# Performance work log

Measured on AMD Instinct MI355X. Metric: run time of the kernel, lower is better.

## Reference

```python
import jax, jax.numpy as jnp
import numpy as np

N_STATIC = 20
N_DYNAMIC = 10
INPUT_DIM = N_STATIC + N_DYNAMIC * 9 + 8  # 118
EMBED = 128
HIDDEN = 1536
HIDDEN2 = 1024
OUT = 128
T = 2048


def setup_inputs() -> dict:
    key = jax.random.key(0)
    ks = jax.random.split(key, 20)
    s = lambda i, shape: jax.random.normal(ks[i], shape, dtype=jnp.float32) * 0.02
    inp = {
        "inputVecs": jax.random.normal(ks[0], (T, INPUT_DIM), dtype=jnp.float32),
        # init_hidden(): randn(num_layers, 1, hidden_dim) -> stored as [2, H]
        "h0": jax.random.normal(ks[1], (2, HIDDEN), dtype=jnp.float32),
        "c0": jax.random.normal(ks[2], (2, HIDDEN), dtype=jnp.float32),
        # LSTM layer 0 (input = INPUT_DIM + EMBED)
        "W_ih0": s(3, (4 * HIDDEN, INPUT_DIM + EMBED)),
        "W_hh0": s(4, (4 * HIDDEN, HIDDEN)),
        "b_ih0": s(5, (4 * HIDDEN,)),
        "b_hh0": s(6, (4 * HIDDEN,)),
        # LSTM layer 1
        "W_ih1": s(7, (4 * HIDDEN, HIDDEN)),
        "W_hh1": s(8, (4 * HIDDEN, HIDDEN)),
        "b_ih1": s(9, (4 * HIDDEN,)),
        "b_hh1": s(10, (4 * HIDDEN,)),
        # hiddenLinear: hidden_dim -> hidden2
        "W_hl": s(11, (HIDDEN2, HIDDEN)),
        "b_hl": s(12, (HIDDEN2,)),
        # linear: hidden2 -> output_dim
        "W_out": s(13, (OUT, HIDDEN2)),
        "b_out": s(14, (OUT,)),
        # map: output_dim -> embed_size
        "W_map": s(15, (EMBED, OUT)),
        "b_map": s(16, (EMBED,)),
    }
    return inp


def _lstm_cell(x, h, c, W_ih, W_hh, b_ih, b_hh):
    # torch gate order: i, f, g, o
    gates = W_ih @ x + b_ih + W_hh @ h + b_hh
    i, f, g, o = jnp.split(gates, 4)
    i = jax.nn.sigmoid(i)
    f = jax.nn.sigmoid(f)
    g = jnp.tanh(g)
    o = jax.nn.sigmoid(o)
    c_new = f * c + i * g
    h_new = o * jnp.tanh(c_new)
    return h_new, c_new


def reference(inputVecs, h0, c0, W_ih0, W_hh0, b_ih0, b_hh0,
              W_ih1, W_hh1, b_ih1, b_hh1,
              W_hl, b_hl, W_out, b_out, W_map, b_map):
    embed0 = jnp.zeros((EMBED,), dtype=inputVecs.dtype)

    def step(carry, x):
        h, c, emb = carry  # h,c: [2, H]; emb: [EMBED]
        xt = jnp.concatenate([x, emb])
        h0n, c0n = _lstm_cell(xt, h[0], c[0], W_ih0, W_hh0, b_ih0, b_hh0)
        h1n, c1n = _lstm_cell(h0n, h[1], c[1], W_ih1, W_hh1, b_ih1, b_hh1)
        # dropout p=0 -> identity; two stacked linears (no nonlinearity, faithful)
        y = W_out @ (W_hl @ h1n + b_hl) + b_out
        y = jax.nn.softmax(y)
        emb_new = W_map @ y + b_map
        return (jnp.stack([h0n, h1n]), jnp.stack([c0n, c1n]), emb_new), y

    _, outputs = jax.lax.scan(step, (h0, c0, embed0), inputVecs)
    return outputs  # [T, OUT]
```

## Files before the change

kernel.cpp:

```cpp
#include <hip/hip_runtime.h>
#include <math.h>
#include <stdint.h>

#define T_STEPS 2048
#define XDIM 118
#define EMBD 128
#define HD 1536
#define NA 96
#define NB 128
#define NBLK (NA + NB + 1)

#define EP_A   0
#define EP_B   128
#define EP_C   256
#define EP_N   320

#define SMEM_BYTES 160048

struct Params {
  const float *x, *h0in, *c0in;
  const float *Wih0, *Whh0, *bih0, *bhh0;
  const float *Wih1, *Whh1, *bih1, *bhh1;
  const float *Whl, *bhl, *Wout, *bout;
  const float *Wfold;
  float *PRE, *Wc, *bc, *h0buf, *h1buf, *ybuf, *PART;
  uint32_t *ep;
  float *out;
};

__device__ __forceinline__ float bf_lo(uint32_t u){ return __uint_as_float(u << 16); }
__device__ __forceinline__ float bf_hi(uint32_t u){ return __uint_as_float(u & 0xffff0000u); }
__device__ __forceinline__ uint32_t packbf(float a, float b){
  uint32_t ua = __float_as_uint(a), ub = __float_as_uint(b);
  ua = (ua + 0x7fffu + ((ua >> 16) & 1u)) >> 16;
  ub = (ub + 0x7fffu + ((ub >> 16) & 1u)) & 0xffff0000u;
  return (ua & 0xffffu) | ub;
}
__device__ __forceinline__ float gload(const float* p){
  return __hip_atomic_load(p, __ATOMIC_RELAXED, __HIP_MEMORY_SCOPE_AGENT);
}
__device__ __forceinline__ void gstore(float* p, float v){
  __hip_atomic_store(p, v, __ATOMIC_RELAXED, __HIP_MEMORY_SCOPE_AGENT);
}
__device__ __forceinline__ uint32_t gloadu(const uint32_t* p){
  return __hip_atomic_load(p, __ATOMIC_RELAXED, __HIP_MEMORY_SCOPE_AGENT);
}
__device__ __forceinline__ void gstoreu(uint32_t* p, uint32_t v){
  __hip_atomic_store(p, v, __ATOMIC_RELAXED, __HIP_MEMORY_SCOPE_AGENT);
}
__device__ __forceinline__ float sigm(float x){ return 1.f / (1.f + __expf(-x)); }

__device__ __forceinline__ void lds_set(volatile uint32_t* f, uint32_t v){
  asm volatile("" ::: "memory");
  *f = v;
  asm volatile("" ::: "memory");
}
__device__ __forceinline__ void lds_wait(volatile uint32_t* f, uint32_t tgt){
  uint32_t n = 0;
  while (*f < tgt){ if (++n > 1000000000u) break; }
  asm volatile("" ::: "memory");
}

__device__ __forceinline__ float asrc(const Params& P, int r, int k){
  if (k < HD) return P.Whh0[(size_t)r * HD + k];
  return P.Wih0[(size_t)r * (XDIM + EMBD) + XDIM + (k - HD)];
}
__device__ void run_A(const Params& P, int bid, uint32_t* smem){
  const int tid = threadIdx.x;
  const int w = tid >> 6, l = tid & 63;
  const int O = bid * 16 + w;
  float* xv = (float*)smem;
  uint2* wl2 = (uint2*)(smem + 1664);
  volatile uint32_t* flg = smem + 18048;
  uint32_t wr[4][8];
  uint32_t wry[4];
#pragma unroll
  for (int g = 0; g < 4; ++g){
    int r = g * HD + O;
#pragma unroll
    for (int p = 0; p < 8; ++p)
      wr[g][p] = packbf(asrc(P, r, 128 * p + 2 * l), asrc(P, r, 128 * p + 2 * l + 1));
#pragma unroll
    for (int q = 0; q < 2; ++q){
      uint2 u;
      u.x = packbf(asrc(P, r, 128 * (8 + 2 * q) + 2 * l), asrc(P, r, 128 * (8 + 2 * q) + 2 * l + 1));
      u.y = packbf(asrc(P, r, 128 * (9 + 2 * q) + 2 * l), asrc(P, r, 128 * (9 + 2 * q) + 2 * l + 1));
      wl2[(q * 4 + g) * 1024 + tid] = u;
    }
    wry[g] = packbf(P.Wfold[(size_t)r * 128 + 2 * l], P.Wfold[(size_t)r * 128 + 2 * l + 1]);
  }
  float cst = P.c0in[O];
  int alive = 1;
  if (tid < 2) flg[tid] = 0u;
  __syncthreads();
  for (int t = 0; t < T_STEPS; ++t){
    const float* pre = P.PRE + (size_t)t * 6144;
    float q0 = pre[O], q1 = pre[HD + O], q2 = pre[2 * HD + O], q3 = pre[3 * HD + O];
    if (w == 0){
      if (alive && t > 0){
        uint32_t n = 0;
        while (1){
          uint32_t v0 = gloadu(P.ep + EP_A + l);
          uint32_t v1 = (l < 32) ? gloadu(P.ep + EP_A + 64 + l) : (uint32_t)t;
          if (__all(v0 >= (uint32_t)t && v1 >= (uint32_t)t)) break;
          if (++n > 5000000u){ alive = 0; break; }
        }
      }
      if (l == 0) lds_set(flg + 0, (uint32_t)t);
    } else {
      lds_wait(flg + 0, (uint32_t)t);
    }
    const float* hp = P.h0buf + (((t & 1) ^ 1) * HD);
    xv[tid] = gload(hp + tid);
    if (tid < 512) xv[1024 + tid] = gload(hp + 1024 + tid);
    __syncthreads();
    float a0 = 0.f, a1 = 0.f, a2 = 0.f, a3 = 0.f;
#pragma unroll
    for (int p = 0; p < 8; ++p){
      float2 x2 = *(const float2*)&xv[128 * p + 2 * l];
      uint32_t u0 = wr[0][p], u1 = wr[1][p], u2 = wr[2][p], u3 = wr[3][p];
      a0 += bf_lo(u0) * x2.x + bf_hi(u0) * x2.y;
      a1 += bf_lo(u1) * x2.x + bf_hi(u1) * x2.y;
      a2 += bf_lo(u2) * x2.x + bf_hi(u2) * x2.y;
      a3 += bf_lo(u3) * x2.x + bf_hi(u3) * x2.y;
    }
#pragma unroll
    for (int q = 0; q < 2; ++q){
      float2 xa = *(const float2*)&xv[128 * (8 + 2 * q) + 2 * l];
      float2 xb = *(const float2*)&xv[128 * (9 + 2 * q) + 2 * l];
      uint2 u0 = wl2[(q * 4 + 0) * 1024 + tid];
      uint2 u1 = wl2[(q * 4 + 1) * 1024 + tid];
      uint2 u2 = wl2[(q * 4 + 2) * 1024 + tid];
      uint2 u3 = wl2[(q * 4 + 3) * 1024 + tid];
      a0 += bf_lo(u0.x) * xa.x + bf_hi(u0.x) * xa.y + bf_lo(u0.y) * xb.x + bf_hi(u0.y) * xb.y;
      a1 += bf_lo(u1.x) * xa.x + bf_hi(u1.x) * xa.y + bf_lo(u1.y) * xb.x + bf_hi(u1.y) * xb.y;
      a2 += bf_lo(u2.x) * xa.x + bf_hi(u2.x) * xa.y + bf_lo(u2.y) * xb.x + bf_hi(u2.y) * xb.y;
      a3 += bf_lo(u3.x) * xa.x + bf_hi(u3.x) * xa.y + bf_lo(u3.y) * xb.x + bf_hi(u3.y) * xb.y;
    }
    if (w == 0){
      if (alive && t > 0){
        uint32_t n = 0;
        while (gloadu(P.ep + EP_C) < (uint32_t)t){
          if (++n > 5000000u){ alive = 0; break; }
        }
      }
      if (l == 0) lds_set(flg + 1, (uint32_t)t);
    } else {
      lds_wait(flg + 1, (uint32_t)t);
    }
    {
      const float* yb = P.ybuf + (((t & 1) ^ 1) * EMBD) + 2 * l;
      float yx = gload(yb), yy = gload(yb + 1);
      a0 += bf_lo(wry[0]) * yx + bf_hi(wry[0]) * yy;
      a1 += bf_lo(wry[1]) * yx + bf_hi(wry[1]) * yy;
      a2 += bf_lo(wry[2]) * yx + bf_hi(wry[2]) * yy;
      a3 += bf_lo(wry[3]) * yx + bf_hi(wry[3]) * yy;
    }
#pragma unroll
    for (int m = 1; m < 64; m <<= 1){
      a0 += __shfl_xor(a0, m, 64);
      a1 += __shfl_xor(a1, m, 64);
      a2 += __shfl_xor(a2, m, 64);
      a3 += __shfl_xor(a3, m, 64);
    }
    float gi = sigm(a0 + q0);
    float gf = sigm(a1 + q1);
    float gg = tanhf(a2 + q2);
    float go = sigm(a3 + q3);
    cst = gf * cst + gi * gg;
    float hn = go * tanhf(cst);
    if (l == 0) gstore(P.h0buf + (t & 1) * HD + O, hn);
    __syncthreads();
    if (tid == 0) gstoreu(P.ep + EP_A + bid, (uint32_t)(t + 1));
  }
}

__device__ __forceinline__ float bsrc(const Params& P, int r, int k){
  if (k < HD) return P.Wih1[(size_t)r * HD + k];
  return P.Whh1[(size_t)r * HD + (k - HD)];
}
__device__ void run_B(const Params& P, int bidb, uint32_t* smem){
  const int tid = threadIdx.x;
  const int w = tid >> 6, l = tid & 63;
  const int base = bidb * 12;
  float* xv = (float*)smem;
  uint2* wl2 = (uint2*)(smem + 3072);
  float* g1 = (float*)(smem + 39936);
  float* c1 = g1 + 48;
  volatile uint32_t* flg = smem + 40008;
  uint32_t wr[3][12];
  float bias[3];
#pragma unroll
  for (int jj = 0; jj < 3; ++jj){
    int idx = 3 * w + jj;
    int g = idx / 12, o = idx % 12;
    int r = g * HD + base + o;
    bias[jj] = P.bih1[r] + P.bhh1[r];
#pragma unroll
    for (int p = 0; p < 12; ++p)
      wr[jj][p] = packbf(bsrc(P, r, 128 * p + 2 * l), bsrc(P, r, 128 * p + 2 * l + 1));
#pragma unroll
    for (int q = 0; q < 6; ++q){
      uint2 u;
      u.x = packbf(bsrc(P, r, 128 * (12 + 2 * q) + 2 * l), bsrc(P, r, 128 * (12 + 2 * q) + 2 * l + 1));
      u.y = packbf(bsrc(P, r, 128 * (13 + 2 * q) + 2 * l), bsrc(P, r, 128 * (13 + 2 * q) + 2 * l + 1));
      wl2[(q * 3 + jj) * 1024 + tid] = u;
    }
  }
  const int jrow = tid >> 2, cpart = tid & 3;
  float wc0 = 0.f, wc1 = 0.f, wc2 = 0.f;
  if (tid < 512){
    const float* wcp = P.Wc + (size_t)jrow * HD + base + cpart * 3;
    wc0 = wcp[0]; wc1 = wcp[1]; wc2 = wcp[2];
  }
  if (tid < 12) c1[12 + tid] = P.c0in[HD + base + tid];
  if (tid < 2) flg[tid] = 0u;
  int alive = 1;
  __syncthreads();
  for (int t = 0; t < T_STEPS; ++t){
    if (w == 0){
      if (alive && t > 0){
        uint32_t n = 0;
        while (gloadu(P.ep + EP_C) < (uint32_t)t){
          if (++n > 5000000u){ alive = 0; break; }
        }
      }
      if (l == 0) lds_set(flg + 0, (uint32_t)t);
    } else {
      lds_wait(flg + 0, (uint32_t)t);
    }
    const float* h1p = P.h1buf + (((t & 1) ^ 1) * HD);
    xv[1536 + tid] = gload(h1p + tid);
    if (tid < 512) xv[2560 + tid] = gload(h1p + 1024 + tid);
    __syncthreads();
    float a0 = 0.f, a1 = 0.f, a2 = 0.f;
#pragma unroll
    for (int q = 0; q < 6; ++q){
      float2 xa = *(const float2*)&xv[128 * (12 + 2 * q) + 2 * l];
      float2 xb = *(const float2*)&xv[128 * (13 + 2 * q) + 2 * l];
      uint2 u0 = wl2[(q * 3 + 0) * 1024 + tid];
      uint2 u1 = wl2[(q * 3 + 1) * 1024 + tid];
      uint2 u2 = wl2[(q * 3 + 2) * 1024 + tid];
      a0 += bf_lo(u0.x) * xa.x + bf_hi(u0.x) * xa.y + bf_lo(u0.y) * xb.x + bf_hi(u0.y) * xb.y;
      a1 += bf_lo(u1.x) * xa.x + bf_hi(u1.x) * xa.y + bf_lo(u1.y) * xb.x + bf_hi(u1.y) * xb.y;
      a2 += bf_lo(u2.x) * xa.x + bf_hi(u2.x) * xa.y + bf_lo(u2.y) * xb.x + bf_hi(u2.y) * xb.y;
    }
    if (w == 0){
      uint32_t tgt = (uint32_t)(t + 1);
      if (alive){
        uint32_t n = 0;
        while (1){
          uint32_t v0 = gloadu(P.ep + EP_A + l);
          uint32_t v1 = (l < 32) ? gloadu(P.ep + EP_A + 64 + l) : tgt;
          if (__all(v0 >= tgt && v1 >= tgt)) break;
          if (++n > 5000000u){ alive = 0; break; }
        }
      }
      if (l == 0) lds_set(flg + 1, tgt);
    } else {
      lds_wait(flg + 1, (uint32_t)(t + 1));
    }
    const float* h0p = P.h0buf + (t & 1) * HD;
    xv[tid] = gload(h0p + tid);
    if (tid < 512) xv[1024 + tid] = gload(h0p + 1024 + tid);
    __syncthreads();
#pragma unroll
    for (int p = 0; p < 12; ++p){
      float2 x2 = *(const float2*)&xv[128 * p + 2 * l];
      uint32_t u0 = wr[0][p], u1 = wr[1][p], u2 = wr[2][p];
      a0 += bf_lo(u0) * x2.x + bf_hi(u0) * x2.y;
      a1 += bf_lo(u1) * x2.x + bf_hi(u1) * x2.y;
      a2 += bf_lo(u2) * x2.x + bf_hi(u2) * x2.y;
    }
#pragma unroll
    for (int m = 1; m < 64; m <<= 1){
      a0 += __shfl_xor(a0, m, 64);
      a1 += __shfl_xor(a1, m, 64);
      a2 += __shfl_xor(a2, m, 64);
    }
    if (l == 0){
      g1[3 * w + 0] = a0 + bias[0];
      g1[3 * w + 1] = a1 + bias[1];
      g1[3 * w + 2] = a2 + bias[2];
    }
    __syncthreads();
    const int par = ((t & 1) ^ 1) * 12, cur = (t & 1) * 12;
    if (tid < 512){
      float h[3], cc[3];
#pragma unroll
      for (int ii = 0; ii < 3; ++ii){
        int o = cpart * 3 + ii;
        float gi = sigm(g1[o]);
        float gf = sigm(g1[12 + o]);
        float gg = tanhf(g1[24 + o]);
        float go = sigm(g1[36 + o]);
        float c = gf * c1[par + o] + gi * gg;
        cc[ii] = c;
        h[ii] = go * tanhf(c);
      }
      float pp = wc0 * h[0] + wc1 * h[1] + wc2 * h[2];
      pp += __shfl_xor(pp, 1, 64);
      pp += __shfl_xor(pp, 2, 64);
      if (cpart == 0) gstore(P.PART + bidb * 128 + jrow, pp);
      if (jrow == 0){
#pragma unroll
        for (int ii = 0; ii < 3; ++ii){
          int o = cpart * 3 + ii;
          c1[cur + o] = cc[ii];
          gstore(P.h1buf + (t & 1) * HD + base + o, h[ii]);
        }
      }
    }
    __syncthreads();
    if (tid == 0) gstoreu(P.ep + EP_B + bidb, (uint32_t)(t + 1));
  }
}

__device__ void run_C(const Params& P, uint32_t* smem){
  const int tid = threadIdx.x;
  float* partred = (float*)smem;
  float* bcs = (float*)(smem + 1024);
  volatile uint32_t* flg = smem + 1152;
  const int w = tid >> 6, l = tid & 63;
  if (tid < 128) bcs[tid] = P.bc[tid];
  if (tid == 0) flg[0] = 0u;
  int alive = 1;
  __syncthreads();
  for (int t = 0; t < T_STEPS; ++t){
    uint32_t tgt = (uint32_t)(t + 1);
    if (w == 0){
      if (alive){
        uint32_t n = 0;
        while (1){
          uint32_t v0 = gloadu(P.ep + EP_B + l);
          uint32_t v1 = gloadu(P.ep + EP_B + 64 + l);
          if (__all(v0 >= tgt && v1 >= tgt)) break;
          if (++n > 5000000u){ alive = 0; break; }
        }
      }
      if (l == 0) lds_set(flg, tgt);
    } else {
      lds_wait(flg, tgt);
    }
    const int j = tid & 127, b8 = tid >> 7;
    float s = 0.f;
#pragma unroll
    for (int i = 0; i < 16; ++i) s += gload(P.PART + (b8 * 16 + i) * 128 + j);
    partred[b8 * 128 + j] = s;
    __syncthreads();
    if (w == 0){
      float lt0 = bcs[l], lt1 = bcs[64 + l];
#pragma unroll
      for (int i = 0; i < 8; ++i){
        lt0 += partred[i * 128 + l];
        lt1 += partred[i * 128 + 64 + l];
      }
      float m = fmaxf(lt0, lt1);
#pragma unroll
      for (int k = 1; k < 64; k <<= 1) m = fmaxf(m, __shfl_xor(m, k, 64));
      float e0 = __expf(lt0 - m), e1 = __expf(lt1 - m);
      float sd = e0 + e1;
#pragma unroll
      for (int k = 1; k < 64; k <<= 1) sd += __shfl_xor(sd, k, 64);
      float inv = 1.f / sd;
      float p0 = e0 * inv, p1 = e1 * inv;
      P.out[(size_t)t * 128 + l] = p0;
      P.out[(size_t)t * 128 + 64 + l] = p1;
      gstore(P.ybuf + (t & 1) * EMBD + l, p0);
      gstore(P.ybuf + (t & 1) * EMBD + 64 + l, p1);
      if (l == 0)
        __hip_atomic_store(P.ep + EP_C, tgt, __ATOMIC_RELEASE, __HIP_MEMORY_SCOPE_AGENT);
    }
  }
}

__global__ __launch_bounds__(1024) void k_lstm(Params P){
  extern __shared__ __align__(16) uint32_t smem[];
  int bid = blockIdx.x;
  if (bid < NA) run_A(P, bid, smem);
  else if (bid < NA + NB) run_B(P, bid - NA, smem);
  else run_C(P, smem);
}

__global__ void k_init(const float* h0in, float* h0buf, float* h1buf, float* ybuf,
                       uint32_t* ep){
  int tid = threadIdx.x;
  for (int i = tid; i < HD; i += 256){
    float a = h0in[i], b = h0in[HD + i];
    h0buf[i] = a; h0buf[HD + i] = a;
    h1buf[i] = b; h1buf[HD + i] = b;
  }
  if (tid < 128){ ybuf[tid] = 0.f; ybuf[128 + tid] = 0.f; }
  for (int i = tid; i < EP_N; i += 256) ep[i] = 0u;
}

__global__ void k_fold(const float* Wih0, const float* Wmap, const float* bmap,
                       float* Wfold, float* bfold){
  __shared__ float we[64 * 128];
  int b = blockIdx.x, tid = threadIdx.x;
  int r0 = b * 64;
  for (int i = tid; i < 64 * 128; i += 256){
    int rr = i >> 7, e = i & 127;
    we[i] = Wih0[(size_t)(r0 + rr) * (XDIM + EMBD) + XDIM + e];
  }
  __syncthreads();
  int j = tid & 127, half = tid >> 7;
  float acc[32];
#pragma unroll
  for (int rr = 0; rr < 32; ++rr) acc[rr] = 0.f;
  for (int e = 0; e < 128; ++e){
    float wv = Wmap[(size_t)e * 128 + j];
#pragma unroll
    for (int rr = 0; rr < 32; ++rr) acc[rr] += we[(half * 32 + rr) * 128 + e] * wv;
  }
  for (int rr = 0; rr < 32; ++rr)
    Wfold[(size_t)(r0 + half * 32 + rr) * 128 + j] = acc[rr];
  if (tid < 64){
    float a = 0.f;
    for (int e = 0; e < 128; ++e) a += we[tid * 128 + e] * bmap[e];
    bfold[r0 + tid] = a;
  }
}

__global__ void k_pre(const float* x, const float* Wih0, const float* bih0, const float* bhh0,
                      const float* bfold, float* PRE){
  int tb = blockIdx.x >> 2;
  int rc = blockIdx.x & 3;
  int tid = threadIdx.x;
  __shared__ float xl[32 * XDIM];
  for (int i = tid; i < 32 * XDIM; i += 256){
    int tt = i / XDIM, k = i % XDIM;
    xl[i] = x[(size_t)(tb * 32 + tt) * XDIM + k];
  }
  __syncthreads();
  for (int rr = 0; rr < 6; ++rr){
    int r = rc * HD + rr * 256 + tid;
    float acc[32];
#pragma unroll
    for (int t = 0; t < 32; ++t) acc[t] = 0.f;
    const float* wrow = Wih0 + (size_t)r * (XDIM + EMBD);
    for (int k = 0; k < XDIM; ++k){
      float wv = wrow[k];
#pragma unroll
      for (int t = 0; t < 32; ++t) acc[t] += wv * xl[t * XDIM + k];
    }
    float bb = bih0[r] + bhh0[r];
    float bf = bfold[r];
    for (int t = 0; t < 32; ++t)
      PRE[(size_t)(tb * 32 + t) * 6144 + r] = acc[t] + bb + ((tb * 32 + t) > 0 ? bf : 0.f);
  }
}

__global__ void k_wc(const float* Whl, const float* Wout, const float* bhl, const float* bout,
                     float* Wc, float* bc){
  if (blockIdx.x == 96){
    int j = threadIdx.x;
    if (j < 128){
      float a = 0.f;
      for (int m = 0; m < 1024; ++m) a += Wout[(size_t)j * 1024 + m] * bhl[m];
      bc[j] = a + bout[j];
    }
    return;
  }
  int kt = blockIdx.x % 6, jt = blockIdx.x / 6;
  __shared__ float wo[8 * 1024];
  int tid = threadIdx.x;
  for (int i = tid; i < 8 * 1024; i += 256) wo[i] = Wout[(size_t)(jt * 8) * 1024 + i];
  __syncthreads();
  int k = kt * 256 + tid;
  float acc[8];
#pragma unroll
  for (int jj = 0; jj < 8; ++jj) acc[jj] = 0.f;
  for (int m = 0; m < 1024; ++m){
    float wl = Whl[(size_t)m * HD + k];
#pragma unroll
    for (int jj = 0; jj < 8; ++jj) acc[jj] += wo[jj * 1024 + m] * wl;
  }
#pragma unroll
  for (int jj = 0; jj < 8; ++jj) Wc[(size_t)(jt * 8 + jj) * HD + k] = acc[jj];
}

__global__ void k_sentinel(float* out){ out[0] = 1.0e6f; }

extern "C" void kernel_launch(void* const* d_in, const int* in_sizes, int n_in,
                              void* d_out, int out_size, void* d_ws, size_t ws_size,
                              hipStream_t stream){
  (void)in_sizes; (void)n_in; (void)out_size;
  const float* x    = (const float*)d_in[0];
  const float* h0in = (const float*)d_in[1];
  const float* c0in = (const float*)d_in[2];
  const float* Wih0 = (const float*)d_in[3];
  const float* Whh0 = (const float*)d_in[4];
  const float* bih0 = (const float*)d_in[5];
  const float* bhh0 = (const float*)d_in[6];
  const float* Wih1 = (const float*)d_in[7];
  const float* Whh1 = (const float*)d_in[8];
  const float* bih1 = (const float*)d_in[9];
  const float* bhh1 = (const float*)d_in[10];
  const float* Whl  = (const float*)d_in[11];
  const float* bhl  = (const float*)d_in[12];
  const float* Wout = (const float*)d_in[13];
  const float* bout = (const float*)d_in[14];
  const float* Wmap = (const float*)d_in[15];
  const float* bmap = (const float*)d_in[16];
  float* out = (float*)d_out;
  float* ws = (float*)d_ws;

  size_t off = 0;
  float* PRE    = ws + off; off += (size_t)T_STEPS * 6144;
  float* Wc     = ws + off; off += 128 * HD;
  float* bc     = ws + off; off += 128;
  float* Wfold  = ws + off; off += (size_t)6144 * 128;
  float* bfold  = ws + off; off += 6144;
  float* h0buf  = ws + off; off += 2 * HD;
  float* h1buf  = ws + off; off += 2 * HD;
  float* ybuf   = ws + off; off += 2 * EMBD;
  float* PART   = ws + off; off += 128 * 128;
  off = (off + 63) & ~(size_t)63;
  uint32_t* ep  = (uint32_t*)(ws + off); off += EP_N;

  if (ws_size < off * sizeof(float) + 1024){
    hipLaunchKernelGGL(k_sentinel, dim3(1), dim3(1), 0, stream, out);
    return;
  }

  (void)hipFuncSetAttribute(reinterpret_cast<const void*>(k_lstm),
                            hipFuncAttributeMaxDynamicSharedMemorySize, SMEM_BYTES);

  hipLaunchKernelGGL(k_init, dim3(1), dim3(256), 0, stream, h0in, h0buf, h1buf, ybuf, ep);
  hipLaunchKernelGGL(k_fold, dim3(96), dim3(256), 0, stream, Wih0, Wmap, bmap, Wfold, bfold);
  hipLaunchKernelGGL(k_pre, dim3(256), dim3(256), 0, stream, x, Wih0, bih0, bhh0, bfold, PRE);
  hipLaunchKernelGGL(k_wc, dim3(97), dim3(256), 0, stream, Whl, Wout, bhl, bout, Wc, bc);

  Params P;
  P.x = x; P.h0in = h0in; P.c0in = c0in;
  P.Wih0 = Wih0; P.Whh0 = Whh0; P.bih0 = bih0; P.bhh0 = bhh0;
  P.Wih1 = Wih1; P.Whh1 = Whh1; P.bih1 = bih1; P.bhh1 = bhh1;
  P.Whl = Whl; P.bhl = bhl; P.Wout = Wout; P.bout = bout;
  P.Wfold = Wfold;
  P.PRE = PRE; P.Wc = Wc; P.bc = bc;
  P.h0buf = h0buf; P.h1buf = h1buf; P.ybuf = ybuf; P.PART = PART;
  P.ep = ep; P.out = out;

  hipLaunchKernelGGL(k_lstm, dim3(NBLK), dim3(1024), SMEM_BYTES, stream, P);
}
```

Baseline: 31.74 ms.

## Remove softmax block; accumulate logits atomically and compute softmax redundantly in A blocks

Removes the dedicated C block that reduced per-block partial logits, applied softmax and published y. B blocks now atomically add their partial logits into a double-buffered, 4-way split accumulator, and every A block reads it and computes the softmax itself before using y. This takes one global synchronisation hop out of the per-step recurrence critical path. The cost is float atomics (non-deterministic summation order), softmax work repeated in every A wave, and a more delicate buffer-reset protocol between B and A.

```diff
diff --git a/kernel.cpp b/kernel.cpp
--- a/kernel.cpp
+++ b/kernel.cpp
@@ -8,12 +8,13 @@
 #define HD 1536
 #define NA 96
 #define NB 128
-#define NBLK (NA + NB + 1)
+#define NBLK (NA + NB)
 
 #define EP_A   0
 #define EP_B   128
-#define EP_C   256
-#define EP_N   320
+#define EP_N   256
+
+#define LA_PAR 512
 
 #define SMEM_BYTES 160048
 
@@ -23,7 +24,7 @@
   const float *Wih1, *Whh1, *bih1, *bhh1;
   const float *Whl, *bhl, *Wout, *bout;
   const float *Wfold;
-  float *PRE, *Wc, *bc, *h0buf, *h1buf, *ybuf, *PART;
+  float *PRE, *Wc, *bc, *h0buf, *h1buf, *logacc;
   uint32_t *ep;
   float *out;
 };
@@ -47,6 +48,9 @@
 }
 __device__ __forceinline__ void gstoreu(uint32_t* p, uint32_t v){
   __hip_atomic_store(p, v, __ATOMIC_RELAXED, __HIP_MEMORY_SCOPE_AGENT);
+}
+__device__ __forceinline__ void gatomic_add(float* p, float v){
+  (void)__hip_atomic_fetch_add(p, v, __ATOMIC_RELAXED, __HIP_MEMORY_SCOPE_AGENT);
 }
 __device__ __forceinline__ float sigm(float x){ return 1.f / (1.f + __expf(-x)); }
 
@@ -137,24 +141,41 @@
       a2 += bf_lo(u2.x) * xa.x + bf_hi(u2.x) * xa.y + bf_lo(u2.y) * xb.x + bf_hi(u2.y) * xb.y;
       a3 += bf_lo(u3.x) * xa.x + bf_hi(u3.x) * xa.y + bf_lo(u3.y) * xb.x + bf_hi(u3.y) * xb.y;
     }
-    if (w == 0){
-      if (alive && t > 0){
-        uint32_t n = 0;
-        while (gloadu(P.ep + EP_C) < (uint32_t)t){
-          if (++n > 5000000u){ alive = 0; break; }
+    if (t > 0){
+      if (w == 0){
+        if (alive){
+          uint32_t n = 0;
+          while (1){
+            uint32_t v0 = gloadu(P.ep + EP_B + l);
+            uint32_t v1 = gloadu(P.ep + EP_B + 64 + l);
+            if (__all(v0 >= (uint32_t)t && v1 >= (uint32_t)t)) break;
+            if (++n > 5000000u){ alive = 0; break; }
+          }
         }
-      }
-      if (l == 0) lds_set(flg + 1, (uint32_t)t);
-    } else {
-      lds_wait(flg + 1, (uint32_t)t);
-    }
-    {
-      const float* yb = P.ybuf + (((t & 1) ^ 1) * EMBD) + 2 * l;
-      float yx = gload(yb), yy = gload(yb + 1);
-      a0 += bf_lo(wry[0]) * yx + bf_hi(wry[0]) * yy;
-      a1 += bf_lo(wry[1]) * yx + bf_hi(wry[1]) * yy;
-      a2 += bf_lo(wry[2]) * yx + bf_hi(wry[2]) * yy;
-      a3 += bf_lo(wry[3]) * yx + bf_hi(wry[3]) * yy;
+        if (l == 0) lds_set(flg + 1, (uint32_t)t);
+      } else {
+        lds_wait(flg + 1, (uint32_t)t);
+      }
+      const float* la = P.logacc + (size_t)(((t & 1) ^ 1) * LA_PAR) + 2 * l;
+      float lt0 = gload(la)     + gload(la + 128) + gload(la + 256) + gload(la + 384);
+      float lt1 = gload(la + 1) + gload(la + 129) + gload(la + 257) + gload(la + 385);
+      float m = fmaxf(lt0, lt1);
+#pragma unroll
+      for (int k = 1; k < 64; k <<= 1) m = fmaxf(m, __shfl_xor(m, k, 64));
+      float e0 = __expf(lt0 - m), e1 = __expf(lt1 - m);
+      float sd = e0 + e1;
+#pragma unroll
+      for (int k = 1; k < 64; k <<= 1) sd += __shfl_xor(sd, k, 64);
+      float inv = 1.f / sd;
+      float y0 = e0 * inv, y1 = e1 * inv;
+      a0 += bf_lo(wry[0]) * y0 + bf_hi(wry[0]) * y1;
+      a1 += bf_lo(wry[1]) * y0 + bf_hi(wry[1]) * y1;
+      a2 += bf_lo(wry[2]) * y0 + bf_hi(wry[2]) * y1;
+      a3 += bf_lo(wry[3]) * y0 + bf_hi(wry[3]) * y1;
+      if (bid == 0 && w == 15){
+        P.out[(size_t)(t - 1) * 128 + 2 * l] = y0;
+        P.out[(size_t)(t - 1) * 128 + 2 * l + 1] = y1;
+      }
     }
 #pragma unroll
     for (int m = 1; m < 64; m <<= 1){
@@ -172,6 +193,30 @@
     if (l == 0) gstore(P.h0buf + (t & 1) * HD + O, hn);
     __syncthreads();
     if (tid == 0) gstoreu(P.ep + EP_A + bid, (uint32_t)(t + 1));
+  }
+  if (bid == 0 && w == 0){
+    if (alive){
+      uint32_t n = 0;
+      while (1){
+        uint32_t v0 = gloadu(P.ep + EP_B + l);
+        uint32_t v1 = gloadu(P.ep + EP_B + 64 + l);
+        if (__all(v0 >= (uint32_t)T_STEPS && v1 >= (uint32_t)T_STEPS)) break;
+        if (++n > 5000000u){ alive = 0; break; }
+      }
+    }
+    const float* la = P.logacc + (size_t)(((T_STEPS & 1) ^ 1) * LA_PAR) + 2 * l;
+    float lt0 = gload(la)     + gload(la + 128) + gload(la + 256) + gload(la + 384);
+    float lt1 = gload(la + 1) + gload(la + 129) + gload(la + 257) + gload(la + 385);
+    float m = fmaxf(lt0, lt1);
+#pragma unroll
+    for (int k = 1; k < 64; k <<= 1) m = fmaxf(m, __shfl_xor(m, k, 64));
+    float e0 = __expf(lt0 - m), e1 = __expf(lt1 - m);
+    float sd = e0 + e1;
+#pragma unroll
+    for (int k = 1; k < 64; k <<= 1) sd += __shfl_xor(sd, k, 64);
+    float inv = 1.f / sd;
+    P.out[(size_t)(T_STEPS - 1) * 128 + 2 * l] = e0 * inv;
+    P.out[(size_t)(T_STEPS - 1) * 128 + 2 * l + 1] = e1 * inv;
   }
 }
 
@@ -213,6 +258,7 @@
     const float* wcp = P.Wc + (size_t)jrow * HD + base + cpart * 3;
     wc0 = wcp[0]; wc1 = wcp[1]; wc2 = wcp[2];
   }
+  float bcv = P.bc[bidb];
   if (tid < 12) c1[12 + tid] = P.c0in[HD + base + tid];
   if (tid < 2) flg[tid] = 0u;
   int alive = 1;
@@ -221,7 +267,10 @@
     if (w == 0){
       if (alive && t > 0){
         uint32_t n = 0;
-        while (gloadu(P.ep + EP_C) < (uint32_t)t){
+        while (1){
+          uint32_t v0 = gloadu(P.ep + EP_B + l);
+          uint32_t v1 = gloadu(P.ep + EP_B + 64 + l);
+          if (__all(v0 >= (uint32_t)t && v1 >= (uint32_t)t)) break;
           if (++n > 5000000u){ alive = 0; break; }
         }
       }
@@ -256,6 +305,9 @@
           if (++n > 5000000u){ alive = 0; break; }
         }
       }
+      if (t > 0 && l < 4)
+        gstore(P.logacc + (size_t)(((t - 1) & 1) * LA_PAR) + l * 128 + bidb,
+               (l == 0) ? bcv : 0.f);
       if (l == 0) lds_set(flg + 1, tgt);
     } else {
       lds_wait(flg + 1, (uint32_t)(t + 1));
@@ -301,7 +353,8 @@
       float pp = wc0 * h[0] + wc1 * h[1] + wc2 * h[2];
       pp += __shfl_xor(pp, 1, 64);
       pp += __shfl_xor(pp, 2, 64);
-      if (cpart == 0) gstore(P.PART + bidb * 128 + jrow, pp);
+      if (cpart == 0)
+        gatomic_add(P.logacc + (size_t)((t & 1) * LA_PAR) + (bidb & 3) * 128 + jrow, pp);
       if (jrow == 0){
 #pragma unroll
         for (int ii = 0; ii < 3; ++ii){
@@ -316,81 +369,25 @@
   }
 }
 
-__device__ void run_C(const Params& P, uint32_t* smem){
-  const int tid = threadIdx.x;
-  float* partred = (float*)smem;
-  float* bcs = (float*)(smem + 1024);
-  volatile uint32_t* flg = smem + 1152;
-  const int w = tid >> 6, l = tid & 63;
-  if (tid < 128) bcs[tid] = P.bc[tid];
-  if (tid == 0) flg[0] = 0u;
-  int alive = 1;
-  __syncthreads();
-  for (int t = 0; t < T_STEPS; ++t){
-    uint32_t tgt = (uint32_t)(t + 1);
-    if (w == 0){
-      if (alive){
-        uint32_t n = 0;
-        while (1){
-          uint32_t v0 = gloadu(P.ep + EP_B + l);
-          uint32_t v1 = gloadu(P.ep + EP_B + 64 + l);
-          if (__all(v0 >= tgt && v1 >= tgt)) break;
-          if (++n > 5000000u){ alive = 0; break; }
-        }
-      }
-      if (l == 0) lds_set(flg, tgt);
-    } else {
-      lds_wait(flg, tgt);
-    }
-    const int j = tid & 127, b8 = tid >> 7;
-    float s = 0.f;
-#pragma unroll
-    for (int i = 0; i < 16; ++i) s += gload(P.PART + (b8 * 16 + i) * 128 + j);
-    partred[b8 * 128 + j] = s;
-    __syncthreads();
-    if (w == 0){
-      float lt0 = bcs[l], lt1 = bcs[64 + l];
-#pragma unroll
-      for (int i = 0; i < 8; ++i){
-        lt0 += partred[i * 128 + l];
-        lt1 += partred[i * 128 + 64 + l];
-      }
-      float m = fmaxf(lt0, lt1);
-#pragma unroll
-      for (int k = 1; k < 64; k <<= 1) m = fmaxf(m, __shfl_xor(m, k, 64));
-      float e0 = __expf(lt0 - m), e1 = __expf(lt1 - m);
-      float sd = e0 + e1;
-#pragma unroll
-      for (int k = 1; k < 64; k <<= 1) sd += __shfl_xor(sd, k, 64);
-      float inv = 1.f / sd;
-      float p0 = e0 * inv, p1 = e1 * inv;
-      P.out[(size_t)t * 128 + l] = p0;
-      P.out[(size_t)t * 128 + 64 + l] = p1;
-      gstore(P.ybuf + (t & 1) * EMBD + l, p0);
-      gstore(P.ybuf + (t & 1) * EMBD + 64 + l, p1);
-      if (l == 0)
-        __hip_atomic_store(P.ep + EP_C, tgt, __ATOMIC_RELEASE, __HIP_MEMORY_SCOPE_AGENT);
-    }
-  }
-}
-
 __global__ __launch_bounds__(1024) void k_lstm(Params P){
   extern __shared__ __align__(16) uint32_t smem[];
   int bid = blockIdx.x;
   if (bid < NA) run_A(P, bid, smem);
-  else if (bid < NA + NB) run_B(P, bid - NA, smem);
-  else run_C(P, smem);
-}
-
-__global__ void k_init(const float* h0in, float* h0buf, float* h1buf, float* ybuf,
-                       uint32_t* ep){
+  else run_B(P, bid - NA, smem);
+}
+
+__global__ void k_init(const float* h0in, const float* bc, float* h0buf, float* h1buf,
+                       float* logacc, uint32_t* ep){
   int tid = threadIdx.x;
   for (int i = tid; i < HD; i += 256){
     float a = h0in[i], b = h0in[HD + i];
     h0buf[i] = a; h0buf[HD + i] = a;
     h1buf[i] = b; h1buf[HD + i] = b;
   }
-  if (tid < 128){ ybuf[tid] = 0.f; ybuf[128 + tid] = 0.f; }
+  for (int i = tid; i < 2 * LA_PAR; i += 256){
+    int s = (i >> 7) & 3, j = i & 127;
+    logacc[i] = (s == 0) ? bc[j] : 0.f;
+  }
   for (int i = tid; i < EP_N; i += 256) ep[i] = 0u;
 }
 
@@ -514,8 +511,7 @@
   float* bfold  = ws + off; off += 6144;
   float* h0buf  = ws + off; off += 2 * HD;
   float* h1buf  = ws + off; off += 2 * HD;
-  float* ybuf   = ws + off; off += 2 * EMBD;
-  float* PART   = ws + off; off += 128 * 128;
+  float* logacc = ws + off; off += 2 * LA_PAR;
   off = (off + 63) & ~(size_t)63;
   uint32_t* ep  = (uint32_t*)(ws + off); off += EP_N;
 
@@ -527,10 +523,10 @@
   (void)hipFuncSetAttribute(reinterpret_cast<const void*>(k_lstm),
                             hipFuncAttributeMaxDynamicSharedMemorySize, SMEM_BYTES);
 
-  hipLaunchKernelGGL(k_init, dim3(1), dim3(256), 0, stream, h0in, h0buf, h1buf, ybuf, ep);
+  hipLaunchKernelGGL(k_wc, dim3(97), dim3(256), 0, stream, Whl, Wout, bhl, bout, Wc, bc);
+  hipLaunchKernelGGL(k_init, dim3(1), dim3(256), 0, stream, h0in, bc, h0buf, h1buf, logacc, ep);
   hipLaunchKernelGGL(k_fold, dim3(96), dim3(256), 0, stream, Wih0, Wmap, bmap, Wfold, bfold);
   hipLaunchKernelGGL(k_pre, dim3(256), dim3(256), 0, stream, x, Wih0, bih0, bhh0, bfold, PRE);
-  hipLaunchKernelGGL(k_wc, dim3(97), dim3(256), 0, stream, Whl, Wout, bhl, bout, Wc, bc);
 
   Params P;
   P.x = x; P.h0in = h0in; P.c0in = c0in;
@@ -539,7 +535,7 @@
   P.Whl = Whl; P.bhl = bhl; P.Wout = Wout; P.bout = bout;
   P.Wfold = Wfold;
   P.PRE = PRE; P.Wc = Wc; P.bc = bc;
-  P.h0buf = h0buf; P.h1buf = h1buf; P.ybuf = ybuf; P.PART = PART;
+  P.h0buf = h0buf; P.h1buf = h1buf; P.logacc = logacc;
   P.ep = ep; P.out = out;
 
   hipLaunchKernelGGL(k_lstm, dim3(NBLK), dim3(1024), SMEM_BYTES, stream, P);
```

Result: slower. 39.41 ms (+24.2%).

## Replace epoch-counter barriers with tagged data records polled directly by consumers

Applied to the files above, without the earlier changes.

Inter-block synchronization in the persistent LSTM kernel switches from separate epoch counters plus data buffers to 16-byte records that carry two values and a step tag. Consumers poll the records themselves with system-coherent vector loads and s_sleep backoff. This removes the counter-then-data round trip and the per-block LDS flag handoff, which shortens the critical path of each timestep. In exchange it relies on 16-byte stores becoming visible atomically, and it writes more global traffic because of the tag padding.

```diff
diff --git a/kernel.cpp b/kernel.cpp
--- a/kernel.cpp
+++ b/kernel.cpp
@@ -10,12 +10,9 @@
 #define NB 128
 #define NBLK (NA + NB + 1)
 
-#define EP_A   0
-#define EP_B   128
-#define EP_C   256
-#define EP_N   320
-
-#define SMEM_BYTES 160048
+#define SMEM_BYTES 160608
+
+typedef uint32_t u32x4 __attribute__((ext_vector_type(4)));
 
 struct Params {
   const float *x, *h0in, *c0in;
@@ -23,8 +20,8 @@
   const float *Wih1, *Whh1, *bih1, *bhh1;
   const float *Whl, *bhl, *Wout, *bout;
   const float *Wfold;
-  float *PRE, *Wc, *bc, *h0buf, *h1buf, *ybuf, *PART;
-  uint32_t *ep;
+  float *PRE, *Wc, *bc;
+  uint4 *h0rec, *h1rec, *partrec, *yrec;
   float *out;
 };
 
@@ -36,29 +33,27 @@
   ub = (ub + 0x7fffu + ((ub >> 16) & 1u)) & 0xffff0000u;
   return (ua & 0xffffu) | ub;
 }
-__device__ __forceinline__ float gload(const float* p){
-  return __hip_atomic_load(p, __ATOMIC_RELAXED, __HIP_MEMORY_SCOPE_AGENT);
-}
-__device__ __forceinline__ void gstore(float* p, float v){
-  __hip_atomic_store(p, v, __ATOMIC_RELAXED, __HIP_MEMORY_SCOPE_AGENT);
-}
-__device__ __forceinline__ uint32_t gloadu(const uint32_t* p){
-  return __hip_atomic_load(p, __ATOMIC_RELAXED, __HIP_MEMORY_SCOPE_AGENT);
-}
-__device__ __forceinline__ void gstoreu(uint32_t* p, uint32_t v){
-  __hip_atomic_store(p, v, __ATOMIC_RELAXED, __HIP_MEMORY_SCOPE_AGENT);
-}
 __device__ __forceinline__ float sigm(float x){ return 1.f / (1.f + __expf(-x)); }
 
-__device__ __forceinline__ void lds_set(volatile uint32_t* f, uint32_t v){
-  asm volatile("" ::: "memory");
-  *f = v;
-  asm volatile("" ::: "memory");
-}
-__device__ __forceinline__ void lds_wait(volatile uint32_t* f, uint32_t tgt){
-  uint32_t n = 0;
-  while (*f < tgt){ if (++n > 1000000000u) break; }
-  asm volatile("" ::: "memory");
+__device__ __forceinline__ u32x4 poll_rec(const uint4* p, uint32_t tag){
+  u32x4 r; uint32_t n = 0;
+  while (1){
+    asm volatile("global_load_dwordx4 %0, %1, off sc0 sc1\n\ts_waitcnt vmcnt(0)"
+                 : "=v"(r) : "v"(p) : "memory");
+    if (r[2] >= tag) break;
+    __builtin_amdgcn_s_sleep(2);
+    if (++n > 2000000u) break;
+  }
+  return r;
+}
+__device__ __forceinline__ u32x4 rec_issue(const uint4* p){
+  u32x4 r;
+  asm volatile("global_load_dwordx4 %0, %1, off sc0 sc1" : "=v"(r) : "v"(p) : "memory");
+  return r;
+}
+__device__ __forceinline__ void st_rec(uint4* p, float a, float b, uint32_t tag){
+  u32x4 v; v[0] = __float_as_uint(a); v[1] = __float_as_uint(b); v[2] = tag; v[3] = 0u;
+  asm volatile("global_store_dwordx4 %0, %1, off sc0 sc1" :: "v"(p), "v"(v) : "memory");
 }
 
 __device__ __forceinline__ float asrc(const Params& P, int r, int k){
@@ -71,7 +66,7 @@
   const int O = bid * 16 + w;
   float* xv = (float*)smem;
   uint2* wl2 = (uint2*)(smem + 1664);
-  volatile uint32_t* flg = smem + 18048;
+  float* h0loc = (float*)(smem + 18048);
   uint32_t wr[4][8];
   uint32_t wry[4];
 #pragma unroll
@@ -90,29 +85,15 @@
     wry[g] = packbf(P.Wfold[(size_t)r * 128 + 2 * l], P.Wfold[(size_t)r * 128 + 2 * l + 1]);
   }
   float cst = P.c0in[O];
-  int alive = 1;
-  if (tid < 2) flg[tid] = 0u;
   __syncthreads();
   for (int t = 0; t < T_STEPS; ++t){
     const float* pre = P.PRE + (size_t)t * 6144;
     float q0 = pre[O], q1 = pre[HD + O], q2 = pre[2 * HD + O], q3 = pre[3 * HD + O];
-    if (w == 0){
-      if (alive && t > 0){
-        uint32_t n = 0;
-        while (1){
-          uint32_t v0 = gloadu(P.ep + EP_A + l);
-          uint32_t v1 = (l < 32) ? gloadu(P.ep + EP_A + 64 + l) : (uint32_t)t;
-          if (__all(v0 >= (uint32_t)t && v1 >= (uint32_t)t)) break;
-          if (++n > 5000000u){ alive = 0; break; }
-        }
-      }
-      if (l == 0) lds_set(flg + 0, (uint32_t)t);
-    } else {
-      lds_wait(flg + 0, (uint32_t)t);
-    }
-    const float* hp = P.h0buf + (((t & 1) ^ 1) * HD);
-    xv[tid] = gload(hp + tid);
-    if (tid < 512) xv[1024 + tid] = gload(hp + 1024 + tid);
+    if (tid < 768){
+      u32x4 r = poll_rec(P.h0rec + ((t & 1) ^ 1) * 768 + tid, (uint32_t)t);
+      xv[2 * tid] = __uint_as_float(r[0]);
+      xv[2 * tid + 1] = __uint_as_float(r[1]);
+    }
     __syncthreads();
     float a0 = 0.f, a1 = 0.f, a2 = 0.f, a3 = 0.f;
 #pragma unroll
@@ -137,24 +118,13 @@
       a2 += bf_lo(u2.x) * xa.x + bf_hi(u2.x) * xa.y + bf_lo(u2.y) * xb.x + bf_hi(u2.y) * xb.y;
       a3 += bf_lo(u3.x) * xa.x + bf_hi(u3.x) * xa.y + bf_lo(u3.y) * xb.x + bf_hi(u3.y) * xb.y;
     }
-    if (w == 0){
-      if (alive && t > 0){
-        uint32_t n = 0;
-        while (gloadu(P.ep + EP_C) < (uint32_t)t){
-          if (++n > 5000000u){ alive = 0; break; }
-        }
-      }
-      if (l == 0) lds_set(flg + 1, (uint32_t)t);
-    } else {
-      lds_wait(flg + 1, (uint32_t)t);
-    }
-    {
-      const float* yb = P.ybuf + (((t & 1) ^ 1) * EMBD) + 2 * l;
-      float yx = gload(yb), yy = gload(yb + 1);
-      a0 += bf_lo(wry[0]) * yx + bf_hi(wry[0]) * yy;
-      a1 += bf_lo(wry[1]) * yx + bf_hi(wry[1]) * yy;
-      a2 += bf_lo(wry[2]) * yx + bf_hi(wry[2]) * yy;
-      a3 += bf_lo(wry[3]) * yx + bf_hi(wry[3]) * yy;
+    if (t > 0){
+      u32x4 r = poll_rec(P.yrec + ((t & 1) ^ 1) * 64 + l, (uint32_t)t);
+      float y0 = __uint_as_float(r[0]), y1 = __uint_as_float(r[1]);
+      a0 += bf_lo(wry[0]) * y0 + bf_hi(wry[0]) * y1;
+      a1 += bf_lo(wry[1]) * y0 + bf_hi(wry[1]) * y1;
+      a2 += bf_lo(wry[2]) * y0 + bf_hi(wry[2]) * y1;
+      a3 += bf_lo(wry[3]) * y0 + bf_hi(wry[3]) * y1;
     }
 #pragma unroll
     for (int m = 1; m < 64; m <<= 1){
@@ -169,9 +139,11 @@
     float go = sigm(a3 + q3);
     cst = gf * cst + gi * gg;
     float hn = go * tanhf(cst);
-    if (l == 0) gstore(P.h0buf + (t & 1) * HD + O, hn);
-    __syncthreads();
-    if (tid == 0) gstoreu(P.ep + EP_A + bid, (uint32_t)(t + 1));
+    if (l == 0) h0loc[w] = hn;
+    __syncthreads();
+    if (tid < 8)
+      st_rec(P.h0rec + (t & 1) * 768 + bid * 8 + tid,
+             h0loc[2 * tid], h0loc[2 * tid + 1], (uint32_t)(t + 1));
   }
 }
 
@@ -186,8 +158,9 @@
   float* xv = (float*)smem;
   uint2* wl2 = (uint2*)(smem + 3072);
   float* g1 = (float*)(smem + 39936);
-  float* c1 = g1 + 48;
-  volatile uint32_t* flg = smem + 40008;
+  float* c1 = (float*)(smem + 39984);
+  float* h1loc = (float*)(smem + 40008);
+  float* plds = (float*)(smem + 40020);
   uint32_t wr[3][12];
   float bias[3];
 #pragma unroll
@@ -214,24 +187,13 @@
     wc0 = wcp[0]; wc1 = wcp[1]; wc2 = wcp[2];
   }
   if (tid < 12) c1[12 + tid] = P.c0in[HD + base + tid];
-  if (tid < 2) flg[tid] = 0u;
-  int alive = 1;
   __syncthreads();
   for (int t = 0; t < T_STEPS; ++t){
-    if (w == 0){
-      if (alive && t > 0){
-        uint32_t n = 0;
-        while (gloadu(P.ep + EP_C) < (uint32_t)t){
-          if (++n > 5000000u){ alive = 0; break; }
-        }
-      }
-      if (l == 0) lds_set(flg + 0, (uint32_t)t);
-    } else {
-      lds_wait(flg + 0, (uint32_t)t);
-    }
-    const float* h1p = P.h1buf + (((t & 1) ^ 1) * HD);
-    xv[1536 + tid] = gload(h1p + tid);
-    if (tid < 512) xv[2560 + tid] = gload(h1p + 1024 + tid);
+    if (tid < 768){
+      u32x4 r = poll_rec(P.h1rec + ((t & 1) ^ 1) * 768 + tid, (uint32_t)t);
+      xv[1536 + 2 * tid] = __uint_as_float(r[0]);
+      xv[1537 + 2 * tid] = __uint_as_float(r[1]);
+    }
     __syncthreads();
     float a0 = 0.f, a1 = 0.f, a2 = 0.f;
 #pragma unroll
@@ -245,24 +207,11 @@
       a1 += bf_lo(u1.x) * xa.x + bf_hi(u1.x) * xa.y + bf_lo(u1.y) * xb.x + bf_hi(u1.y) * xb.y;
       a2 += bf_lo(u2.x) * xa.x + bf_hi(u2.x) * xa.y + bf_lo(u2.y) * xb.x + bf_hi(u2.y) * xb.y;
     }
-    if (w == 0){
-      uint32_t tgt = (uint32_t)(t + 1);
-      if (alive){
-        uint32_t n = 0;
-        while (1){
-          uint32_t v0 = gloadu(P.ep + EP_A + l);
-          uint32_t v1 = (l < 32) ? gloadu(P.ep + EP_A + 64 + l) : tgt;
-          if (__all(v0 >= tgt && v1 >= tgt)) break;
-          if (++n > 5000000u){ alive = 0; break; }
-        }
-      }
-      if (l == 0) lds_set(flg + 1, tgt);
-    } else {
-      lds_wait(flg + 1, (uint32_t)(t + 1));
-    }
-    const float* h0p = P.h0buf + (t & 1) * HD;
-    xv[tid] = gload(h0p + tid);
-    if (tid < 512) xv[1024 + tid] = gload(h0p + 1024 + tid);
+    if (tid < 768){
+      u32x4 r = poll_rec(P.h0rec + (t & 1) * 768 + tid, (uint32_t)(t + 1));
+      xv[2 * tid] = __uint_as_float(r[0]);
+      xv[2 * tid + 1] = __uint_as_float(r[1]);
+    }
     __syncthreads();
 #pragma unroll
     for (int p = 0; p < 12; ++p){
@@ -301,59 +250,71 @@
       float pp = wc0 * h[0] + wc1 * h[1] + wc2 * h[2];
       pp += __shfl_xor(pp, 1, 64);
       pp += __shfl_xor(pp, 2, 64);
-      if (cpart == 0) gstore(P.PART + bidb * 128 + jrow, pp);
+      if (cpart == 0) plds[jrow] = pp;
       if (jrow == 0){
 #pragma unroll
         for (int ii = 0; ii < 3; ++ii){
           int o = cpart * 3 + ii;
           c1[cur + o] = cc[ii];
-          gstore(P.h1buf + (t & 1) * HD + base + o, h[ii]);
+          h1loc[o] = h[ii];
         }
       }
     }
     __syncthreads();
-    if (tid == 0) gstoreu(P.ep + EP_B + bidb, (uint32_t)(t + 1));
+    uint32_t tg = (uint32_t)(t + 1);
+    if (tid < 6)
+      st_rec(P.h1rec + (t & 1) * 768 + bidb * 6 + tid,
+             h1loc[2 * tid], h1loc[2 * tid + 1], tg);
+    else if (tid >= 64 && tid < 128){
+      int r = tid - 64;
+      st_rec(P.partrec + (size_t)(t & 1) * 8192 + bidb * 64 + r,
+             plds[2 * r], plds[2 * r + 1], tg);
+    }
   }
 }
 
 __device__ void run_C(const Params& P, uint32_t* smem){
   const int tid = threadIdx.x;
   float* partred = (float*)smem;
-  float* bcs = (float*)(smem + 1024);
-  volatile uint32_t* flg = smem + 1152;
+  float* bcs = (float*)(smem + 2048);
   const int w = tid >> 6, l = tid & 63;
+  const int g8 = tid >> 6, j2 = tid & 63;
   if (tid < 128) bcs[tid] = P.bc[tid];
-  if (tid == 0) flg[0] = 0u;
-  int alive = 1;
   __syncthreads();
   for (int t = 0; t < T_STEPS; ++t){
-    uint32_t tgt = (uint32_t)(t + 1);
+    const uint4* base = P.partrec + (size_t)(t & 1) * 8192;
+    uint32_t tg = (uint32_t)(t + 1);
+    u32x4 rec[8];
+    uint32_t done = 0, n = 0;
+    while (done != 0xFFu){
+#pragma unroll
+      for (int k = 0; k < 8; ++k)
+        if (!(done & (1u << k))) rec[k] = rec_issue(base + (size_t)(8 * g8 + k) * 64 + j2);
+      asm volatile("s_waitcnt vmcnt(0)" ::: "memory");
+      __builtin_amdgcn_sched_barrier(0);
+#pragma unroll
+      for (int k = 0; k < 8; ++k)
+        if (rec[k][2] >= tg) done |= (1u << k);
+      if (done != 0xFFu){
+        __builtin_amdgcn_s_sleep(2);
+        if (++n > 2000000u) break;
+      }
+    }
+    float s0 = 0.f, s1 = 0.f;
+#pragma unroll
+    for (int k = 0; k < 8; ++k){
+      s0 += __uint_as_float(rec[k][0]);
+      s1 += __uint_as_float(rec[k][1]);
+    }
+    partred[g8 * 128 + 2 * j2] = s0;
+    partred[g8 * 128 + 2 * j2 + 1] = s1;
+    __syncthreads();
     if (w == 0){
-      if (alive){
-        uint32_t n = 0;
-        while (1){
-          uint32_t v0 = gloadu(P.ep + EP_B + l);
-          uint32_t v1 = gloadu(P.ep + EP_B + 64 + l);
-          if (__all(v0 >= tgt && v1 >= tgt)) break;
-          if (++n > 5000000u){ alive = 0; break; }
-        }
-      }
-      if (l == 0) lds_set(flg, tgt);
-    } else {
-      lds_wait(flg, tgt);
-    }
-    const int j = tid & 127, b8 = tid >> 7;
-    float s = 0.f;
-#pragma unroll
-    for (int i = 0; i < 16; ++i) s += gload(P.PART + (b8 * 16 + i) * 128 + j);
-    partred[b8 * 128 + j] = s;
-    __syncthreads();
-    if (w == 0){
-      float lt0 = bcs[l], lt1 = bcs[64 + l];
-#pragma unroll
-      for (int i = 0; i < 8; ++i){
-        lt0 += partred[i * 128 + l];
-        lt1 += partred[i * 128 + 64 + l];
+      float lt0 = bcs[2 * l], lt1 = bcs[2 * l + 1];
+#pragma unroll
+      for (int g = 0; g < 16; ++g){
+        lt0 += partred[g * 128 + 2 * l];
+        lt1 += partred[g * 128 + 2 * l + 1];
       }
       float m = fmaxf(lt0, lt1);
 #pragma unroll
@@ -363,13 +324,10 @@
 #pragma unroll
       for (int k = 1; k < 64; k <<= 1) sd += __shfl_xor(sd, k, 64);
       float inv = 1.f / sd;
-      float p0 = e0 * inv, p1 = e1 * inv;
-      P.out[(size_t)t * 128 + l] = p0;
-      P.out[(size_t)t * 128 + 64 + l] = p1;
-      gstore(P.ybuf + (t & 1) * EMBD + l, p0);
-      gstore(P.ybuf + (t & 1) * EMBD + 64 + l, p1);
-      if (l == 0)
-        __hip_atomic_store(P.ep + EP_C, tgt, __ATOMIC_RELEASE, __HIP_MEMORY_SCOPE_AGENT);
+      float y0 = e0 * inv, y1 = e1 * inv;
+      P.out[(size_t)t * 128 + 2 * l] = y0;
+      P.out[(size_t)t * 128 + 2 * l + 1] = y1;
+      st_rec(P.yrec + (t & 1) * 64 + l, y0, y1, tg);
     }
   }
 }
@@ -382,16 +340,20 @@
   else run_C(P, smem);
 }
 
-__global__ void k_init(const float* h0in, float* h0buf, float* h1buf, float* ybuf,
-                       uint32_t* ep){
+__global__ void k_init(const float* h0in, uint4* h0rec, uint4* h1rec,
+                       uint4* partrec, uint4* yrec){
   int tid = threadIdx.x;
-  for (int i = tid; i < HD; i += 256){
-    float a = h0in[i], b = h0in[HD + i];
-    h0buf[i] = a; h0buf[HD + i] = a;
-    h1buf[i] = b; h1buf[HD + i] = b;
-  }
-  if (tid < 128){ ybuf[tid] = 0.f; ybuf[128 + tid] = 0.f; }
-  for (int i = tid; i < EP_N; i += 256) ep[i] = 0u;
+  for (int i = tid; i < 768; i += 256){
+    uint4 r0; r0.x = __float_as_uint(h0in[2 * i]); r0.y = __float_as_uint(h0in[2 * i + 1]);
+    r0.z = 0u; r0.w = 0u;
+    h0rec[i] = r0; h0rec[768 + i] = r0;
+    uint4 r1; r1.x = __float_as_uint(h0in[HD + 2 * i]); r1.y = __float_as_uint(h0in[HD + 2 * i + 1]);
+    r1.z = 0u; r1.w = 0u;
+    h1rec[i] = r1; h1rec[768 + i] = r1;
+  }
+  uint4 z; z.x = 0u; z.y = 0u; z.z = 0u; z.w = 0u;
+  for (int i = tid; i < 16384; i += 256) partrec[i] = z;
+  for (int i = tid; i < 128; i += 256) yrec[i] = z;
 }
 
 __global__ void k_fold(const float* Wih0, const float* Wmap, const float* bmap,
@@ -512,12 +474,11 @@
   float* bc     = ws + off; off += 128;
   float* Wfold  = ws + off; off += (size_t)6144 * 128;
   float* bfold  = ws + off; off += 6144;
-  float* h0buf  = ws + off; off += 2 * HD;
-  float* h1buf  = ws + off; off += 2 * HD;
-  float* ybuf   = ws + off; off += 2 * EMBD;
-  float* PART   = ws + off; off += 128 * 128;
-  off = (off + 63) & ~(size_t)63;
-  uint32_t* ep  = (uint32_t*)(ws + off); off += EP_N;
+  off = (off + 3) & ~(size_t)3;
+  uint4* h0rec   = (uint4*)(ws + off); off += 2 * 768 * 4;
+  uint4* h1rec   = (uint4*)(ws + off); off += 2 * 768 * 4;
+  uint4* partrec = (uint4*)(ws + off); off += 2 * 8192 * 4;
+  uint4* yrec    = (uint4*)(ws + off); off += 2 * 64 * 4;
 
   if (ws_size < off * sizeof(float) + 1024){
     hipLaunchKernelGGL(k_sentinel, dim3(1), dim3(1), 0, stream, out);
@@ -527,7 +488,7 @@
   (void)hipFuncSetAttribute(reinterpret_cast<const void*>(k_lstm),
                             hipFuncAttributeMaxDynamicSharedMemorySize, SMEM_BYTES);
 
-  hipLaunchKernelGGL(k_init, dim3(1), dim3(256), 0, stream, h0in, h0buf, h1buf, ybuf, ep);
+  hipLaunchKernelGGL(k_init, dim3(1), dim3(256), 0, stream, h0in, h0rec, h1rec, partrec, yrec);
   hipLaunchKernelGGL(k_fold, dim3(96), dim3(256), 0, stream, Wih0, Wmap, bmap, Wfold, bfold);
   hipLaunchKernelGGL(k_pre, dim3(256), dim3(256), 0, stream, x, Wih0, bih0, bhh0, bfold, PRE);
   hipLaunchKernelGGL(k_wc, dim3(97), dim3(256), 0, stream, Whl, Wout, bhl, bout, Wc, bc);
@@ -539,8 +500,8 @@
   P.Whl = Whl; P.bhl = bhl; P.Wout = Wout; P.bout = bout;
   P.Wfold = Wfold;
   P.PRE = PRE; P.Wc = Wc; P.bc = bc;
-  P.h0buf = h0buf; P.h1buf = h1buf; P.ybuf = ybuf; P.PART = PART;
-  P.ep = ep; P.out = out;
+  P.h0rec = h0rec; P.h1rec = h1rec; P.partrec = partrec; P.yrec = yrec;
+  P.out = out;
 
   hipLaunchKernelGGL(k_lstm, dim3(NBLK), dim3(1024), SMEM_BYTES, stream, P);
 }
```

Result: faster. 27.81 ms (-12.4%).
